# Optimization experiments

Measured on AMD Instinct MI355X. Metric: run time of the kernel, lower is better.

## Reference

```python
import jax, jax.numpy as jnp
import numpy as np

N_USERS = 100000
N_ITEMS = 50000
N_NODES = N_USERS + N_ITEMS
DIM = 64
N_EDGES = 4800000
N_LAYERS = 3
BATCH = 131072


def setup_inputs() -> dict:
    key = jax.random.key(0)
    ks = jax.random.split(key, 7)
    # Xavier-uniform-ish init for embeddings
    bound_u = np.sqrt(6.0 / (N_USERS + DIM)).astype(np.float32)
    bound_i = np.sqrt(6.0 / (N_ITEMS + DIM)).astype(np.float32)
    user_emb = jax.random.uniform(ks[0], (N_USERS, DIM), jnp.float32, -bound_u, bound_u)
    item_emb = jax.random.uniform(ks[1], (N_ITEMS, DIM), jnp.float32, -bound_i, bound_i)
    edge_src = jax.random.randint(ks[2], (N_EDGES,), 0, N_NODES, jnp.int32)
    edge_dst = jax.random.randint(ks[3], (N_EDGES,), 0, N_NODES, jnp.int32)
    # normalized adjacency values (D^-1/2 A D^-1/2) ~ small positive weights
    edge_weight = jax.random.uniform(ks[4], (N_EDGES,), jnp.float32) * 0.1
    users = jax.random.randint(ks[5], (BATCH,), 0, N_USERS, jnp.int32)
    items = jax.random.randint(ks[6], (BATCH,), 0, N_ITEMS, jnp.int32)
    return {"user_emb": user_emb, "item_emb": item_emb,
            "edge_src": edge_src, "edge_dst": edge_dst, "edge_weight": edge_weight,
            "users": users, "items": items}


def _spmm(edge_src, edge_dst, edge_weight, x):
    # out[dst] += w * x[src]  (sparse adjacency @ x)
    msgs = x[edge_src] * edge_weight[:, None]  # [E, D]
    return jax.ops.segment_sum(msgs, edge_dst, num_segments=N_NODES)


def reference(user_emb, item_emb, edge_src, edge_dst, edge_weight, users, items):
    # LightGCN.computer(): multi-hop propagation, mean over layer outputs
    all_emb = jnp.concatenate([user_emb, item_emb], axis=0)  # [N, D]
    acc = all_emb
    for _ in range(N_LAYERS):
        all_emb = _spmm(edge_src, edge_dst, edge_weight, all_emb)
        acc = acc + all_emb
    light_out = acc / jnp.float32(N_LAYERS + 1)  # mean over stacked layers
    users_emb = light_out[users]                  # all_users[users]
    items_emb = light_out[N_USERS + items]        # all_items[items]
    gamma = jnp.sum(users_emb * items_emb, axis=1)
    return gamma
```

## Files before the change

kernel.cpp:

```cpp
#include <hip/hip_runtime.h>
#include <hip/hip_fp16.h>

#define N_USERS 100000
#define N_ITEMS 50000
#define N_NODES 150000
#define DIM 64
#define N_EDGES 4800000
#define N_LAYERS 3
#define BATCH 131072
#define NELEM (N_NODES * DIM)

#define NB 320
#define DPB 469
#define CAP 16000

__global__ void cursor_init_kernel(int* __restrict__ cursor) {
    int i = threadIdx.x + blockIdx.x * blockDim.x;
    if (i < NB) cursor[i] = i * CAP;
}

#define SCT_T 1024
#define SCT_EPT 8
#define SCT_TILE (SCT_T * SCT_EPT)
__global__ __launch_bounds__(SCT_T) void bscatter_kernel(
        const int* __restrict__ esrc,
        const int* __restrict__ edst,
        const float* __restrict__ ew,
        int* __restrict__ bucket_cursor,
        int2* __restrict__ stage) {
    __shared__ int cnt[NB];
    __shared__ int runbase[NB];
    const int tid = threadIdx.x;
    const int tile0 = blockIdx.x * SCT_TILE;

    for (int i = tid; i < NB; i += SCT_T) cnt[i] = 0;
    __syncthreads();

    int   src[SCT_EPT], bkt[SCT_EPT], dl[SCT_EPT];
    float w[SCT_EPT];
    #pragma unroll
    for (int k = 0; k < SCT_EPT; ++k) {
        int e = tile0 + k * SCT_T + tid;
        if (e < N_EDGES) {
            int d = edst[e];
            src[k] = esrc[e];
            w[k]   = ew[e];
            bkt[k] = d / DPB;
            dl[k]  = d - bkt[k] * DPB;
            atomicAdd(&cnt[bkt[k]], 1);
        } else bkt[k] = -1;
    }
    __syncthreads();
    for (int i = tid; i < NB; i += SCT_T)
        runbase[i] = cnt[i] ? atomicAdd(&bucket_cursor[i], cnt[i]) : 0;
    __syncthreads();
    for (int i = tid; i < NB; i += SCT_T) cnt[i] = 0;
    __syncthreads();
    #pragma unroll
    for (int k = 0; k < SCT_EPT; ++k) {
        if (bkt[k] >= 0) {
            int r   = atomicAdd(&cnt[bkt[k]], 1);
            int pos = runbase[bkt[k]] + r;
            if (pos < (bkt[k] + 1) * CAP)
                stage[pos] = make_int2(src[k] | (dl[k] << 18), __float_as_int(w[k]));
        }
    }
}

#define SRT_T 1024
__global__ __launch_bounds__(SRT_T) void bsort_kernel(
        const int* __restrict__ bucket_cursor,
        const int2* __restrict__ stage,
        int2* __restrict__ edge_sorted,
        int* __restrict__ rowbeg,
        int* __restrict__ rowcnt) {
    __shared__ int cnt[DPB];
    __shared__ int s[SRT_T];
    const int b   = blockIdx.x;
    const int tid = threadIdx.x;
    const int base = b * CAP;
    const int n    = min(bucket_cursor[b] - base, CAP);
    const int d0   = b * DPB;
    const int nd   = min(DPB, N_NODES - d0);

    for (int i = tid; i < nd; i += SRT_T) cnt[i] = 0;
    __syncthreads();
    for (int j = tid; j < n; j += SRT_T)
        atomicAdd(&cnt[stage[base + j].x >> 18], 1);
    __syncthreads();
    int v = (tid < nd) ? cnt[tid] : 0;
    s[tid] = v;
    __syncthreads();
    for (int off = 1; off < SRT_T; off <<= 1) {
        int t = (tid >= off) ? s[tid - off] : 0;
        __syncthreads();
        s[tid] += t;
        __syncthreads();
    }
    if (tid < nd) {
        int excl = s[tid] - v;
        rowbeg[d0 + tid] = base + excl;
        rowcnt[d0 + tid] = v;
        cnt[tid]         = excl;
    }
    __syncthreads();
    for (int j = tid; j < n; j += SRT_T) {
        int2 e  = stage[base + j];
        int  dl = e.x >> 18;
        int pos = base + atomicAdd(&cnt[dl], 1);
        __half  hw = __float2half_rn(__int_as_float(e.y));
        __half2 h2 = __halves2half2(hw, hw);
        edge_sorted[pos] = make_int2(e.x & 0x3FFFF, *(int*)&h2);
    }
}

__global__ void init_kernel(const float* __restrict__ user_emb,
                            const float* __restrict__ item_emb,
                            __half* __restrict__ x0) {
    int i = blockIdx.x * blockDim.x + threadIdx.x;
    const int n4 = NELEM / 4;
    if (i >= n4) return;
    const int nu4 = (N_USERS * DIM) / 4;
    float4 v = (i < nu4) ? ((const float4*)user_emb)[i]
                         : ((const float4*)item_emb)[i - nu4];
    __half2 h01 = __floats2half2_rn(v.x, v.y);
    __half2 h23 = __floats2half2_rn(v.z, v.w);
    uint2 st;
    st.x = *(unsigned int*)&h01;
    st.y = *(unsigned int*)&h23;
    ((uint2*)x0)[i] = st;
}

__device__ __forceinline__ void pk_acc(const uint4& g, int wbits,
                                       __half2& s0, __half2& s1,
                                       __half2& s2, __half2& s3) {
    __half2 w2 = *(const __half2*)&wbits;
    s0 = __hfma2(w2, *(const __half2*)&g.x, s0);
    s1 = __hfma2(w2, *(const __half2*)&g.y, s1);
    s2 = __hfma2(w2, *(const __half2*)&g.z, s2);
    s3 = __hfma2(w2, *(const __half2*)&g.w, s3);
}

__global__ __launch_bounds__(256) void spmm_kernel(
        const int* __restrict__ rowbeg,
        const int* __restrict__ rowcnt,
        const int2* __restrict__ es,
        const __half* __restrict__ x,
        __half* __restrict__ out,
        const __half* __restrict__ a0,
        const __half* __restrict__ a1,
        const __half* __restrict__ a2) {
    int gtid = blockIdx.x * blockDim.x + threadIdx.x;
    int node = gtid >> 6;
    int lane = threadIdx.x & 63;
    if (node >= N_NODES) return;
    const int g  = lane >> 3;
    const int sl = lane & 7;
    int beg = rowbeg[node];
    int end = beg + rowcnt[node];
    __half2 s0 = __halves2half2(__float2half(0.f), __float2half(0.f));
    __half2 s1 = s0, s2 = s0, s3 = s0;
    int j = beg;

    int2 ea = make_int2(0, 0), eb = make_int2(0, 0);
    bool have = (j + 16 <= end);
    if (have) { ea = es[j + g]; eb = es[j + 8 + g]; }
    while (have) {
        int jn = j + 16;
        bool haven = (jn + 16 <= end);
        int2 na = make_int2(0, 0), nb = make_int2(0, 0);
        if (haven) { na = es[jn + g]; nb = es[jn + 8 + g]; }
        uint4 ga = *((const uint4*)(x + (size_t)ea.x * DIM) + sl);
        uint4 gb = *((const uint4*)(x + (size_t)eb.x * DIM) + sl);
        pk_acc(ga, ea.y, s0, s1, s2, s3);
        pk_acc(gb, eb.y, s0, s1, s2, s3);
        ea = na; eb = nb; j = jn; have = haven;
    }
    while (j < end) {
        int e = j + g;
        if (e < end) {
            int2 et = es[e];
            uint4 gt = *((const uint4*)(x + (size_t)et.x * DIM) + sl);
            pk_acc(gt, et.y, s0, s1, s2, s3);
        }
        j += 8;
    }
    #pragma unroll
    for (int off = 8; off <= 32; off <<= 1) {
        int t0 = __shfl_xor(*(int*)&s0, off, 64);
        int t1 = __shfl_xor(*(int*)&s1, off, 64);
        int t2 = __shfl_xor(*(int*)&s2, off, 64);
        int t3 = __shfl_xor(*(int*)&s3, off, 64);
        s0 = __hadd2(s0, *(__half2*)&t0);
        s1 = __hadd2(s1, *(__half2*)&t1);
        s2 = __hadd2(s2, *(__half2*)&t2);
        s3 = __hadd2(s3, *(__half2*)&t3);
    }
    if (g == 0) {
        if (a0) {
            size_t ro = (size_t)node * DIM;
            uint4 v0 = *((const uint4*)(a0 + ro) + sl);
            uint4 v1 = *((const uint4*)(a1 + ro) + sl);
            uint4 v2 = *((const uint4*)(a2 + ro) + sl);
            s0 = __hadd2(s0, __hadd2(*(__half2*)&v0.x, __hadd2(*(__half2*)&v1.x, *(__half2*)&v2.x)));
            s1 = __hadd2(s1, __hadd2(*(__half2*)&v0.y, __hadd2(*(__half2*)&v1.y, *(__half2*)&v2.y)));
            s2 = __hadd2(s2, __hadd2(*(__half2*)&v0.z, __hadd2(*(__half2*)&v1.z, *(__half2*)&v2.z)));
            s3 = __hadd2(s3, __hadd2(*(__half2*)&v0.w, __hadd2(*(__half2*)&v1.w, *(__half2*)&v2.w)));
        }
        uint4 st;
        st.x = *(unsigned int*)&s0;
        st.y = *(unsigned int*)&s1;
        st.z = *(unsigned int*)&s2;
        st.w = *(unsigned int*)&s3;
        *(((uint4*)(out + (size_t)node * DIM)) + sl) = st;
    }
}

__global__ void dot_kernel(const __half* __restrict__ xs,
                           const int* __restrict__ users,
                           const int* __restrict__ items,
                           float* __restrict__ out) {
    int gtid = blockIdx.x * blockDim.x + threadIdx.x;
    int b    = gtid >> 6;
    int lane = threadIdx.x & 63;
    if (b >= BATCH) return;
    int half = lane >> 5;
    int sl   = lane & 31;
    int row  = half ? (items[b] + N_USERS) : users[b];
    float2 f = __half22float2(*(const __half2*)(xs + (size_t)row * DIM + 2 * sl));
    float ox = __shfl_xor(f.x, 32, 64);
    float oy = __shfl_xor(f.y, 32, 64);
    float p = f.x * ox + f.y * oy;
    p += __shfl_xor(p, 16, 64);
    p += __shfl_xor(p, 8, 64);
    p += __shfl_xor(p, 4, 64);
    p += __shfl_xor(p, 2, 64);
    p += __shfl_xor(p, 1, 64);
    if (lane == 0) out[b] = p * 0.0625f;
}

extern "C" void kernel_launch(void* const* d_in, const int* in_sizes, int n_in,
                              void* d_out, int out_size, void* d_ws, size_t ws_size,
                              hipStream_t stream) {
    const float* user_emb = (const float*)d_in[0];
    const float* item_emb = (const float*)d_in[1];
    const int*   esrc     = (const int*)d_in[2];
    const int*   edst     = (const int*)d_in[3];
    const float* ew       = (const float*)d_in[4];
    const int*   users    = (const int*)d_in[5];
    const int*   items    = (const int*)d_in[6];
    float*       out      = (float*)d_out;

    char*   base = (char*)d_ws;
    __half* x0 = (__half*)base;
    __half* x1 = x0 + NELEM;
    __half* x2 = x1 + NELEM;
    __half* xs = x2 + NELEM;
    int2*   stage = (int2*)base;
    int2*   edge_sorted = (int2*)(base + (size_t)4 * NELEM * 2);
    int*    rowbeg = (int*)(edge_sorted + (size_t)NB * CAP);
    int*    rowcnt = rowbeg + N_NODES;
    int*    cursor = rowcnt + N_NODES;

    const int BLK = 256;
    dim3 gridElem((NELEM / 4 + BLK - 1) / BLK);
    dim3 gridSpmm(((size_t)N_NODES * 64 + BLK - 1) / BLK);
    dim3 gridDot(((size_t)BATCH * 64 + BLK - 1) / BLK);
    dim3 gridSct((N_EDGES + SCT_TILE - 1) / SCT_TILE);

    cursor_init_kernel<<<1, 512, 0, stream>>>(cursor);
    bscatter_kernel<<<gridSct, SCT_T, 0, stream>>>(esrc, edst, ew, cursor, stage);
    bsort_kernel<<<NB, SRT_T, 0, stream>>>(cursor, stage, edge_sorted, rowbeg, rowcnt);

    init_kernel<<<gridElem, BLK, 0, stream>>>(user_emb, item_emb, x0);

    spmm_kernel<<<gridSpmm, BLK, 0, stream>>>(rowbeg, rowcnt, edge_sorted, x0, x1,
                                              nullptr, nullptr, nullptr);
    spmm_kernel<<<gridSpmm, BLK, 0, stream>>>(rowbeg, rowcnt, edge_sorted, x1, x2,
                                              nullptr, nullptr, nullptr);
    spmm_kernel<<<gridSpmm, BLK, 0, stream>>>(rowbeg, rowcnt, edge_sorted, x2, xs,
                                              x0, x1, x2);

    dot_kernel<<<gridDot, BLK, 0, stream>>>(xs, users, items, out);
}
```

Before: 512.7 us.

## Stage scatter through shared memory, register-cache sort edges, add nontemporal loads

The bucket scatter now converts weights to half early, prefix-scans the per-bucket counts and stages edges in shared memory, so each block's global writes to the stage buffer go out grouped by bucket instead of scattered. The bucket sort keeps its edges in registers between the counting and placement passes, which removes the second read of the stage buffer. Nontemporal loads and stores are added to streaming accesses in the sort, init and spmm kernels so they do not evict the gathered embedding rows from cache. The costs are more shared memory per scatter block, which may lower occupancy, and the risk that nontemporal hints hurt accesses that actually reuse data.

```diff
diff --git a/kernel.cpp b/kernel.cpp
--- a/kernel.cpp
+++ b/kernel.cpp
@@ -14,12 +14,27 @@
 #define DPB 469
 #define CAP 16000
 
+typedef int vint4 __attribute__((ext_vector_type(4)));
+
+__device__ __forceinline__ int2 ntld_i2(const int2* p) {
+    long v = __builtin_nontemporal_load((const long*)p);
+    int2 r; r.x = (int)v; r.y = (int)(v >> 32); return r;
+}
+__device__ __forceinline__ uint4 ntld_u4(const void* p) {
+    vint4 t = __builtin_nontemporal_load((const vint4*)p);
+    uint4 r; r.x = t.x; r.y = t.y; r.z = t.z; r.w = t.w; return r;
+}
+__device__ __forceinline__ void ntst_u4(void* p, uint4 v) {
+    vint4 t; t.x = v.x; t.y = v.y; t.z = v.z; t.w = v.w;
+    __builtin_nontemporal_store(t, (vint4*)p);
+}
+
 __global__ void cursor_init_kernel(int* __restrict__ cursor) {
     int i = threadIdx.x + blockIdx.x * blockDim.x;
     if (i < NB) cursor[i] = i * CAP;
 }
 
-#define SCT_T 1024
+#define SCT_T 512
 #define SCT_EPT 8
 #define SCT_TILE (SCT_T * SCT_EPT)
 __global__ __launch_bounds__(SCT_T) void bscatter_kernel(
@@ -28,46 +43,74 @@
         const float* __restrict__ ew,
         int* __restrict__ bucket_cursor,
         int2* __restrict__ stage) {
-    __shared__ int cnt[NB];
-    __shared__ int runbase[NB];
+    __shared__ int  cnt[NB];
+    __shared__ int  lexcl[NB];
+    __shared__ int  runbase[NB];
+    __shared__ int  sscan[512];
+    __shared__ int2 sedge[SCT_TILE];
+    __shared__ int  saddr[SCT_TILE];
     const int tid = threadIdx.x;
     const int tile0 = blockIdx.x * SCT_TILE;
+    const int nthis = min(SCT_TILE, N_EDGES - tile0);
 
     for (int i = tid; i < NB; i += SCT_T) cnt[i] = 0;
     __syncthreads();
 
-    int   src[SCT_EPT], bkt[SCT_EPT], dl[SCT_EPT];
-    float w[SCT_EPT];
+    int srcdl[SCT_EPT], bkt[SCT_EPT], wh2[SCT_EPT];
     #pragma unroll
     for (int k = 0; k < SCT_EPT; ++k) {
         int e = tile0 + k * SCT_T + tid;
+        bkt[k] = -1;
         if (e < N_EDGES) {
-            int d = edst[e];
-            src[k] = esrc[e];
-            w[k]   = ew[e];
-            bkt[k] = d / DPB;
-            dl[k]  = d - bkt[k] * DPB;
-            atomicAdd(&cnt[bkt[k]], 1);
-        } else bkt[k] = -1;
-    }
-    __syncthreads();
-    for (int i = tid; i < NB; i += SCT_T)
-        runbase[i] = cnt[i] ? atomicAdd(&bucket_cursor[i], cnt[i]) : 0;
+            int   d = __builtin_nontemporal_load(edst + e);
+            int   s = __builtin_nontemporal_load(esrc + e);
+            float w = __builtin_nontemporal_load(ew + e);
+            int b  = d / DPB;
+            int dl = d - b * DPB;
+            bkt[k]   = b;
+            srcdl[k] = s | (dl << 18);
+            __half  hw = __float2half_rn(w);
+            __half2 h2 = __halves2half2(hw, hw);
+            wh2[k] = *(int*)&h2;
+            atomicAdd(&cnt[b], 1);
+        }
+    }
+    __syncthreads();
+    int v = (tid < NB) ? cnt[tid] : 0;
+    sscan[tid] = v;
+    __syncthreads();
+    for (int off = 1; off < 512; off <<= 1) {
+        int t = (tid >= off) ? sscan[tid - off] : 0;
+        __syncthreads();
+        sscan[tid] += t;
+        __syncthreads();
+    }
+    if (tid < NB) {
+        lexcl[tid]   = sscan[tid] - v;
+        runbase[tid] = atomicAdd(&bucket_cursor[tid], v);
+    }
     __syncthreads();
     for (int i = tid; i < NB; i += SCT_T) cnt[i] = 0;
     __syncthreads();
     #pragma unroll
     for (int k = 0; k < SCT_EPT; ++k) {
         if (bkt[k] >= 0) {
-            int r   = atomicAdd(&cnt[bkt[k]], 1);
-            int pos = runbase[bkt[k]] + r;
-            if (pos < (bkt[k] + 1) * CAP)
-                stage[pos] = make_int2(src[k] | (dl[k] << 18), __float_as_int(w[k]));
-        }
+            int r    = atomicAdd(&cnt[bkt[k]], 1);
+            int slot = lexcl[bkt[k]] + r;
+            int pos  = runbase[bkt[k]] + r;
+            sedge[slot] = make_int2(srcdl[k], wh2[k]);
+            saddr[slot] = (pos < (bkt[k] + 1) * CAP) ? pos : -1;
+        }
+    }
+    __syncthreads();
+    for (int t = tid; t < nthis; t += SCT_T) {
+        int pos = saddr[t];
+        if (pos >= 0) stage[pos] = sedge[t];
     }
 }
 
 #define SRT_T 1024
+#define SRT_EPT 16
 __global__ __launch_bounds__(SRT_T) void bsort_kernel(
         const int* __restrict__ bucket_cursor,
         const int2* __restrict__ stage,
@@ -75,7 +118,7 @@
         int* __restrict__ rowbeg,
         int* __restrict__ rowcnt) {
     __shared__ int cnt[DPB];
-    __shared__ int s[SRT_T];
+    __shared__ int s[512];
     const int b   = blockIdx.x;
     const int tid = threadIdx.x;
     const int base = b * CAP;
@@ -85,16 +128,23 @@
 
     for (int i = tid; i < nd; i += SRT_T) cnt[i] = 0;
     __syncthreads();
-    for (int j = tid; j < n; j += SRT_T)
-        atomicAdd(&cnt[stage[base + j].x >> 18], 1);
+    int2 ed[SRT_EPT];
+    #pragma unroll
+    for (int k = 0; k < SRT_EPT; ++k) {
+        int j = tid + k * SRT_T;
+        if (j < n) {
+            ed[k] = ntld_i2(stage + base + j);
+            atomicAdd(&cnt[ed[k].x >> 18], 1);
+        }
+    }
     __syncthreads();
     int v = (tid < nd) ? cnt[tid] : 0;
-    s[tid] = v;
-    __syncthreads();
-    for (int off = 1; off < SRT_T; off <<= 1) {
-        int t = (tid >= off) ? s[tid - off] : 0;
+    if (tid < 512) s[tid] = v;
+    __syncthreads();
+    for (int off = 1; off < 512; off <<= 1) {
+        int t = (tid >= off && tid < 512) ? s[tid - off] : 0;
         __syncthreads();
-        s[tid] += t;
+        if (tid < 512) s[tid] += t;
         __syncthreads();
     }
     if (tid < nd) {
@@ -104,13 +154,14 @@
         cnt[tid]         = excl;
     }
     __syncthreads();
-    for (int j = tid; j < n; j += SRT_T) {
-        int2 e  = stage[base + j];
-        int  dl = e.x >> 18;
-        int pos = base + atomicAdd(&cnt[dl], 1);
-        __half  hw = __float2half_rn(__int_as_float(e.y));
-        __half2 h2 = __halves2half2(hw, hw);
-        edge_sorted[pos] = make_int2(e.x & 0x3FFFF, *(int*)&h2);
+    #pragma unroll
+    for (int k = 0; k < SRT_EPT; ++k) {
+        int j = tid + k * SRT_T;
+        if (j < n) {
+            int dl  = ed[k].x >> 18;
+            int pos = base + atomicAdd(&cnt[dl], 1);
+            edge_sorted[pos] = make_int2(ed[k].x & 0x3FFFF, ed[k].y);
+        }
     }
 }
 
@@ -121,10 +172,11 @@
     const int n4 = NELEM / 4;
     if (i >= n4) return;
     const int nu4 = (N_USERS * DIM) / 4;
-    float4 v = (i < nu4) ? ((const float4*)user_emb)[i]
-                         : ((const float4*)item_emb)[i - nu4];
-    __half2 h01 = __floats2half2_rn(v.x, v.y);
-    __half2 h23 = __floats2half2_rn(v.z, v.w);
+    uint4 raw = (i < nu4) ? ntld_u4((const float4*)user_emb + i)
+                          : ntld_u4((const float4*)item_emb + (i - nu4));
+    float4 vf = *(float4*)&raw;
+    __half2 h01 = __floats2half2_rn(vf.x, vf.y);
+    __half2 h23 = __floats2half2_rn(vf.z, vf.w);
     uint2 st;
     st.x = *(unsigned int*)&h01;
     st.y = *(unsigned int*)&h23;
@@ -164,12 +216,12 @@
 
     int2 ea = make_int2(0, 0), eb = make_int2(0, 0);
     bool have = (j + 16 <= end);
-    if (have) { ea = es[j + g]; eb = es[j + 8 + g]; }
+    if (have) { ea = ntld_i2(es + j + g); eb = ntld_i2(es + j + 8 + g); }
     while (have) {
         int jn = j + 16;
         bool haven = (jn + 16 <= end);
         int2 na = make_int2(0, 0), nb = make_int2(0, 0);
-        if (haven) { na = es[jn + g]; nb = es[jn + 8 + g]; }
+        if (haven) { na = ntld_i2(es + jn + g); nb = ntld_i2(es + jn + 8 + g); }
         uint4 ga = *((const uint4*)(x + (size_t)ea.x * DIM) + sl);
         uint4 gb = *((const uint4*)(x + (size_t)eb.x * DIM) + sl);
         pk_acc(ga, ea.y, s0, s1, s2, s3);
@@ -179,7 +231,7 @@
     while (j < end) {
         int e = j + g;
         if (e < end) {
-            int2 et = es[e];
+            int2 et = ntld_i2(es + e);
             uint4 gt = *((const uint4*)(x + (size_t)et.x * DIM) + sl);
             pk_acc(gt, et.y, s0, s1, s2, s3);
         }
@@ -199,9 +251,9 @@
     if (g == 0) {
         if (a0) {
             size_t ro = (size_t)node * DIM;
-            uint4 v0 = *((const uint4*)(a0 + ro) + sl);
-            uint4 v1 = *((const uint4*)(a1 + ro) + sl);
-            uint4 v2 = *((const uint4*)(a2 + ro) + sl);
+            uint4 v0 = ntld_u4((const uint4*)(a0 + ro) + sl);
+            uint4 v1 = ntld_u4((const uint4*)(a1 + ro) + sl);
+            uint4 v2 = ntld_u4((const uint4*)(a2 + ro) + sl);
             s0 = __hadd2(s0, __hadd2(*(__half2*)&v0.x, __hadd2(*(__half2*)&v1.x, *(__half2*)&v2.x)));
             s1 = __hadd2(s1, __hadd2(*(__half2*)&v0.y, __hadd2(*(__half2*)&v1.y, *(__half2*)&v2.y)));
             s2 = __hadd2(s2, __hadd2(*(__half2*)&v0.z, __hadd2(*(__half2*)&v1.z, *(__half2*)&v2.z)));
@@ -212,7 +264,7 @@
         st.y = *(unsigned int*)&s1;
         st.z = *(unsigned int*)&s2;
         st.w = *(unsigned int*)&s3;
-        *(((uint4*)(out + (size_t)node * DIM)) + sl) = st;
+        ntst_u4((uint4*)(out + (size_t)node * DIM) + sl, st);
     }
 }
 
```

New measurement: 506.2 us. Within noise of the previous version (-1.3%).
